# Performance work log

Measured on AMD Instinct MI355X. Metric: run time of the kernel, lower is better.

## Reference

```python
import jax, jax.numpy as jnp
import numpy as np

THRESHOLD = 1.0
THRESHOLD_LOW = -1.0
WINDOW = 1.0  # sinabs global `window` multiplier -> surrogate window = threshold * 1.0
BATCH = 32


@jax.custom_vjp
def threshold_subtract(v):
    # sinabs ThresholdSubtract.forward: (v > 0) * floor(v / threshold)
    return jnp.where(v > 0, jnp.floor(v / THRESHOLD), jnp.zeros_like(v))


def _ts_fwd(v):
    return threshold_subtract(v), v


def _ts_bwd(v, g):
    # surrogate gradient: pass grad where v >= threshold - window, scaled by 1/threshold
    mask = (v >= (THRESHOLD - THRESHOLD * WINDOW)).astype(g.dtype)
    return (g * mask / THRESHOLD,)


threshold_subtract.defvjp(_ts_fwd, _ts_bwd)


def setup_inputs() -> dict:
    key = jax.random.key(0)
    # (batch*time, features) = (32*1024, 1024); scale so membrane crosses threshold sometimes
    data = jax.random.normal(key, (32 * 1024, 1024), dtype=jnp.float32) * 0.8 + 0.3
    return {"data": data}


def reference(data):
    F = data.shape[-1]
    # SpikingLayer: (B*T, F) -> (B, T, F) -> (T, B, F)
    x = data.reshape(BATCH, -1, F).transpose(1, 0, 2)
    state0 = jnp.zeros(x.shape[1:], dtype=x.dtype)
    act0 = jnp.zeros_like(state0)

    def step(carry, xt):
        state, act = carry
        # membrane_reset=False: subtract membrane_subtract (== threshold) per spike
        state = xt + state - act * THRESHOLD
        # lower-bound clamp at threshold_low
        state = jax.nn.relu(state - THRESHOLD_LOW) + THRESHOLD_LOW
        act = threshold_subtract(state)
        return (state, act), act

    _, spikes = jax.lax.scan(step, (state0, act0), x)  # (T, B, F)
    # back to (B*T, F)
    return spikes.transpose(1, 0, 2).reshape(-1, F)
```

## Files before the change

kernel.cpp:

```cpp
#include <hip/hip_runtime.h>


constexpr int T = 1024;
constexpr int F = 1024;
constexpr int DEPTH = 32;
constexpr int CH = DEPTH * 64;
constexpr int RING = 5;

#define WAITVM(N) asm volatile("s_waitcnt vmcnt(" #N ")" ::: "memory")
#define LGKM0()   asm volatile("s_waitcnt lgkmcnt(0)" ::: "memory")
#define SFENCE()  __builtin_amdgcn_sched_barrier(0)

__global__ __launch_bounds__(64) void iaf_kernel(const float* __restrict__ x,
                                                 float* __restrict__ out) {
    __shared__ float ring[RING * CH];
    __shared__ float outT[2 * CH];

    const int lane = threadIdx.x;
    const int b = blockIdx.x >> 4;
    const int f0 = (blockIdx.x & 15) * 64;

    const size_t base = ((size_t)b * T) * F + f0;
    const float* __restrict__ p = x + base;
    float* __restrict__ qo = out + base;

    const int lrow = lane >> 4;
    const int lcol = (lane & 15) * 4;

    float s = 0.0f, a = 0.0f;

    auto issue = [&](int k, int rb) {
        float* lb = &ring[rb * CH];
#pragma unroll
        for (int r = 0; r < 8; ++r) {
            const float* g = p + (size_t)(k * DEPTH + r * 4 + lrow) * F + lcol;
            __builtin_amdgcn_global_load_lds(
                (const __attribute__((address_space(1))) void*)g,
                (__attribute__((address_space(3))) void*)(lb + r * 256),
                16, 0, 0);
        }
        SFENCE();
    };

    auto compute = [&](int k, int rb) {
        const float* lb = &ring[rb * CH];
        float* ot = &outT[(k & 1) * CH];
        float xv[DEPTH];
#pragma unroll
        for (int i = 0; i < DEPTH; ++i) xv[i] = lb[i * 64 + lane];
#pragma unroll
        for (int i = 0; i < DEPTH; ++i) {
            s = (xv[i] + s) - a;
            s = fmaxf(s + 1.0f, 0.0f) - 1.0f;
            a = floorf(fmaxf(s, 0.0f));
            ot[i * 64 + lane] = a;
        }
        LGKM0();
        SFENCE();
#pragma unroll
        for (int j = 0; j < 8; ++j) {
            const int row = j * 4 + lrow;
            const float4 v = *(const float4*)&ot[row * 64 + lcol];
            *(float4*)(qo + (size_t)(k * DEPTH + row) * F + lcol) = v;
        }
        SFENCE();
    };

    issue(0, 0); issue(1, 1); issue(2, 2); issue(3, 3);

    WAITVM(24); issue(4, 4); compute(0, 0);
    WAITVM(32); issue(5, 0); compute(1, 1);
    WAITVM(40); issue(6, 1); compute(2, 2);
    WAITVM(40); issue(7, 2); compute(3, 3);

    int bc = 4, bl = 3;
    for (int c = 4; c <= 27; ++c) {
        WAITVM(40);
        issue(c + 4, bl);
        compute(c, bc);
        bc = (bc == RING - 1) ? 0 : bc + 1;
        bl = (bl == RING - 1) ? 0 : bl + 1;
    }

    WAITVM(40); compute(28, 3);
    WAITVM(40); compute(29, 4);
    WAITVM(32); compute(30, 0);
    WAITVM(24); compute(31, 1);
}

extern "C" void kernel_launch(void* const* d_in, const int* in_sizes, int n_in,
                              void* d_out, int out_size, void* d_ws, size_t ws_size,
                              hipStream_t stream) {
    const float* x = (const float*)d_in[0];
    float* out = (float*)d_out;
    iaf_kernel<<<dim3(512), dim3(64), 0, stream>>>(x, out);
}
```

Before: 51.84 us.

## Split loader and compute into separate waves with an eight-slot LDS ring

Adds a dedicated producer wave that streams input chunks into an eight-deep LDS ring via async global-to-LDS loads, while a consumer wave runs the recurrence, coordinated by workgroup barriers. Output is written directly per lane per row instead of being staged through an LDS transpose buffer. The clamp/floor arithmetic is slightly reformulated to share a term. This aims to decouple load latency from the serial recurrence, at the cost of barrier synchronization, larger LDS use and narrower stores.

```diff
diff --git a/kernel.cpp b/kernel.cpp
--- a/kernel.cpp
+++ b/kernel.cpp
@@ -4,88 +4,76 @@
 constexpr int T = 1024;
 constexpr int F = 1024;
 constexpr int DEPTH = 32;
+constexpr int NC = T / DEPTH;
 constexpr int CH = DEPTH * 64;
-constexpr int RING = 5;
+constexpr int RING = 8;
 
 #define WAITVM(N) asm volatile("s_waitcnt vmcnt(" #N ")" ::: "memory")
-#define LGKM0()   asm volatile("s_waitcnt lgkmcnt(0)" ::: "memory")
 #define SFENCE()  __builtin_amdgcn_sched_barrier(0)
+#define BAR()     do { SFENCE(); __builtin_amdgcn_s_barrier(); SFENCE(); } while (0)
 
-__global__ __launch_bounds__(64) void iaf_kernel(const float* __restrict__ x,
-                                                 float* __restrict__ out) {
+__global__ __launch_bounds__(128) void iaf_kernel(const float* __restrict__ x,
+                                                  float* __restrict__ out) {
     __shared__ float ring[RING * CH];
-    __shared__ float outT[2 * CH];
 
-    const int lane = threadIdx.x;
+    const int lane = threadIdx.x & 63;
+    const int wave = threadIdx.x >> 6;
     const int b = blockIdx.x >> 4;
     const int f0 = (blockIdx.x & 15) * 64;
+    const size_t base = ((size_t)b * T) * F + f0;
 
-    const size_t base = ((size_t)b * T) * F + f0;
-    const float* __restrict__ p = x + base;
-    float* __restrict__ qo = out + base;
+    if (wave == 1) {
+        const float* __restrict__ p = x + base;
+        const int lrow = lane >> 4;
+        const int lcol = (lane & 15) * 4;
 
-    const int lrow = lane >> 4;
-    const int lcol = (lane & 15) * 4;
+        auto issue = [&](int k) {
+            float* lb = &ring[(k & 7) * CH];
+#pragma unroll
+            for (int r = 0; r < 8; ++r) {
+                const float* g = p + (size_t)(k * DEPTH + r * 4 + lrow) * F + lcol;
+                __builtin_amdgcn_global_load_lds(
+                    (const __attribute__((address_space(1))) void*)g,
+                    (__attribute__((address_space(3))) void*)(lb + r * 256),
+                    16, 0, 0);
+            }
+            SFENCE();
+        };
 
-    float s = 0.0f, a = 0.0f;
-
-    auto issue = [&](int k, int rb) {
-        float* lb = &ring[rb * CH];
+        issue(0); issue(1); issue(2); issue(3); issue(4); issue(5); issue(6);
+        WAITVM(48);
+        BAR();
+        for (int c = 0; c <= 24; ++c) {
+            issue(c + 7);
+            WAITVM(48);
+            BAR();
+        }
+        WAITVM(40); BAR();
+        WAITVM(32); BAR();
+        WAITVM(24); BAR();
+        WAITVM(16); BAR();
+        WAITVM(8);  BAR();
+        WAITVM(0);  BAR();
+    } else {
+        float* __restrict__ q = out + base + lane;
+        float s = 0.0f, a = 0.0f;
+        for (int c = 0; c < NC; ++c) {
+            BAR();
+            const float* lb = &ring[(c & 7) * CH];
+            float xv[DEPTH];
 #pragma unroll
-        for (int r = 0; r < 8; ++r) {
-            const float* g = p + (size_t)(k * DEPTH + r * 4 + lrow) * F + lcol;
-            __builtin_amdgcn_global_load_lds(
-                (const __attribute__((address_space(1))) void*)g,
-                (__attribute__((address_space(3))) void*)(lb + r * 256),
-                16, 0, 0);
+            for (int i = 0; i < DEPTH; ++i) xv[i] = lb[i * 64 + lane];
+#pragma unroll
+            for (int i = 0; i < DEPTH; ++i) {
+                const float s1 = (xv[i] + s) - a;
+                const float t2 = s1 + 1.0f;
+                s = fmaxf(t2, 0.0f) - 1.0f;
+                a = floorf(fmaxf(t2, 1.0f) - 1.0f);
+                q[(size_t)(c * DEPTH + i) * F] = a;
+            }
+            SFENCE();
         }
-        SFENCE();
-    };
-
-    auto compute = [&](int k, int rb) {
-        const float* lb = &ring[rb * CH];
-        float* ot = &outT[(k & 1) * CH];
-        float xv[DEPTH];
-#pragma unroll
-        for (int i = 0; i < DEPTH; ++i) xv[i] = lb[i * 64 + lane];
-#pragma unroll
-        for (int i = 0; i < DEPTH; ++i) {
-            s = (xv[i] + s) - a;
-            s = fmaxf(s + 1.0f, 0.0f) - 1.0f;
-            a = floorf(fmaxf(s, 0.0f));
-            ot[i * 64 + lane] = a;
-        }
-        LGKM0();
-        SFENCE();
-#pragma unroll
-        for (int j = 0; j < 8; ++j) {
-            const int row = j * 4 + lrow;
-            const float4 v = *(const float4*)&ot[row * 64 + lcol];
-            *(float4*)(qo + (size_t)(k * DEPTH + row) * F + lcol) = v;
-        }
-        SFENCE();
-    };
-
-    issue(0, 0); issue(1, 1); issue(2, 2); issue(3, 3);
-
-    WAITVM(24); issue(4, 4); compute(0, 0);
-    WAITVM(32); issue(5, 0); compute(1, 1);
-    WAITVM(40); issue(6, 1); compute(2, 2);
-    WAITVM(40); issue(7, 2); compute(3, 3);
-
-    int bc = 4, bl = 3;
-    for (int c = 4; c <= 27; ++c) {
-        WAITVM(40);
-        issue(c + 4, bl);
-        compute(c, bc);
-        bc = (bc == RING - 1) ? 0 : bc + 1;
-        bl = (bl == RING - 1) ? 0 : bl + 1;
     }
-
-    WAITVM(40); compute(28, 3);
-    WAITVM(40); compute(29, 4);
-    WAITVM(32); compute(30, 0);
-    WAITVM(24); compute(31, 1);
 }
 
 extern "C" void kernel_launch(void* const* d_in, const int* in_sizes, int n_in,
@@ -93,5 +81,5 @@
                               hipStream_t stream) {
     const float* x = (const float*)d_in[0];
     float* out = (float*)d_out;
-    iaf_kernel<<<dim3(512), dim3(64), 0, stream>>>(x, out);
+    iaf_kernel<<<dim3(512), dim3(128), 0, stream>>>(x, out);
 }
```

Result: faster. 46.69 us (-9.9%).
